# Optimization experiments

Measured on AMD Instinct MI355X. Metric: run time of the kernel, lower is better.

Reference implementation:

```python
import jax, jax.numpy as jnp
import numpy as np

VOCAB = 32000
HIDDEN = 1024
BATCH = 8
SEQ = 512


def setup_inputs() -> dict:
    key = jax.random.key(0)
    ks = jax.random.split(key, 6)
    scale = 1.0 / np.sqrt(HIDDEN)
    return {
        "sequence_ids": jax.random.randint(ks[0], (BATCH, SEQ), 0, VOCAB, dtype=jnp.int64),
        "W_out": jax.random.normal(ks[1], (HIDDEN, VOCAB), dtype=jnp.float32) * scale,
        "b_out": jax.random.normal(ks[2], (VOCAB,), dtype=jnp.float32) * 0.01,
        "Wx": jax.random.normal(ks[3], (HIDDEN, 4 * HIDDEN), dtype=jnp.float32) * scale,
        "Wh": jax.random.normal(ks[4], (HIDDEN, 4 * HIDDEN), dtype=jnp.float32) * scale,
        "b_lstm": jax.random.normal(ks[5], (4 * HIDDEN,), dtype=jnp.float32) * 0.01,
    }


def _lstm(emb, Wx, Wh, b):
    # emb: [B, S, H]; scan over time with carry (h, c) of shape [B, H]
    B, S, H = emb.shape
    # Precompute input projections for all timesteps in one big GEMM.
    x_gates = jnp.einsum("bsh,hg->bsg", emb, Wx) + b  # [B, S, 4H]

    def step(carry, xg_t):
        h, c = carry
        gates = xg_t + h @ Wh  # [B, 4H]
        i, f, g, o = jnp.split(gates, 4, axis=-1)
        i = jax.nn.sigmoid(i)
        f = jax.nn.sigmoid(f)
        g = jnp.tanh(g)
        o = jax.nn.sigmoid(o)
        c = f * c + i * g
        h = o * jnp.tanh(c)
        return (h, c), h

    h0 = jnp.zeros((B, H), dtype=emb.dtype)
    c0 = jnp.zeros((B, H), dtype=emb.dtype)
    (_, _), hs = jax.lax.scan(step, (h0, c0), jnp.swapaxes(x_gates, 0, 1))
    return jnp.swapaxes(hs, 0, 1)  # [B, S, H]


def reference(sequence_ids, W_out, b_out, Wx, Wh, b_lstm):
    # Weight-tied embedding lookup: W_out is [H, V]; take columns -> [B, S, H]
    emb = W_out.T[sequence_ids]
    hs = _lstm(emb, Wx, Wh, b_lstm)  # [B, S, H]
    logits = jnp.einsum("bsh,hv->bsv", hs, W_out) + b_out  # [B, S, V]
    return logits
```

## Files before the change

kernel.cpp:

```cpp
#include <hip/hip_runtime.h>

#define VOCAB  32000
#define HIDDEN 1024
#define BATCH  8
#define SEQ    512
#define GDIM   4096

typedef short bf16x8 __attribute__((ext_vector_type(8)));
typedef float f32x4  __attribute__((ext_vector_type(4)));

__device__ __forceinline__ unsigned short f2bf(float f) {
    unsigned int u = __float_as_uint(f);
    u += 0x7fff + ((u >> 16) & 1);
    return (unsigned short)(u >> 16);
}

__device__ __forceinline__ float sigmoidf_(float x) {
    return 1.0f / (1.0f + expf(-x));
}

__global__ __launch_bounds__(256) void convert_bf16(const float* __restrict__ in,
                                                    unsigned short* __restrict__ out,
                                                    int n4) {
    int i = blockIdx.x * 256 + threadIdx.x;
    if (i < n4) {
        float4 v = ((const float4*)in)[i];
        ushort4 o;
        o.x = f2bf(v.x); o.y = f2bf(v.y); o.z = f2bf(v.z); o.w = f2bf(v.w);
        ((ushort4*)out)[i] = o;
    }
}

__global__ __launch_bounds__(256) void gather_emb(const int* __restrict__ ids,
                                                  const float* __restrict__ W_out,
                                                  unsigned short* __restrict__ emb) {
    int r = blockIdx.x;
    int s = r >> 3, b = r & 7;
    int v = ids[b * SEQ + s];
    #pragma unroll
    for (int i = 0; i < 4; ++i) {
        int h = threadIdx.x + i * 256;
        emb[r * HIDDEN + h] = f2bf(W_out[(size_t)h * VOCAB + v]);
    }
}

__global__ __launch_bounds__(256) void transpose_wh(const float* __restrict__ Wh,
                                                    unsigned short* __restrict__ whT) {
    __shared__ unsigned short tile[32][33];
    const int j0 = blockIdx.x * 32;
    const int k0 = blockIdx.y * 32;
    const int c = threadIdx.x & 31;
    const int r = threadIdx.x >> 5;
    #pragma unroll
    for (int i = 0; i < 4; ++i) {
        int rr = r + i * 8;
        tile[rr][c] = f2bf(Wh[(size_t)(k0 + rr) * GDIM + j0 + c]);
    }
    __syncthreads();
    #pragma unroll
    for (int i = 0; i < 4; ++i) {
        int rr = r + i * 8;
        whT[(size_t)(j0 + rr) * HIDDEN + k0 + c] = tile[c][rr];
    }
}

__global__ __launch_bounds__(256) void gemm_bf16_bias(
        const unsigned short* __restrict__ A,
        const unsigned short* __restrict__ B,
        const float* __restrict__ bias,
        float* __restrict__ C,
        int M, int N, int K) {
    __shared__ __attribute__((aligned(16))) unsigned short As[128 * 40];
    __shared__ __attribute__((aligned(16))) unsigned short Bs[128 * 40];

    const int tid  = threadIdx.x;
    const int lane = tid & 63;
    const int wave = tid >> 6;
    const int wm = wave >> 1, wn = wave & 1;
    const int quad = lane >> 4, r16 = lane & 15;
    const int m0 = blockIdx.y * 128, n0 = blockIdx.x * 128;

    f32x4 acc[4][4] = {};

    for (int k0 = 0; k0 < K; k0 += 32) {
        #pragma unroll
        for (int i = 0; i < 2; ++i) {
            int c = tid + 256 * i;
            int m = c >> 2, kc = (c & 3) * 8;
            uint4 v = *(const uint4*)(A + (size_t)(m0 + m) * K + k0 + kc);
            *(uint4*)(As + m * 40 + kc) = v;
        }
        #pragma unroll
        for (int i = 0; i < 2; ++i) {
            int c = tid + 256 * i;
            int k = c >> 4, nc = (c & 15) * 8;
            uint4 v = *(const uint4*)(B + (size_t)(k0 + k) * N + n0 + nc);
            union { uint4 q; unsigned short s[8]; } u; u.q = v;
            #pragma unroll
            for (int j = 0; j < 8; ++j) Bs[(nc + j) * 40 + k] = u.s[j];
        }
        __syncthreads();

        bf16x8 af[4], bfr[4];
        #pragma unroll
        for (int mi = 0; mi < 4; ++mi)
            af[mi] = *(const bf16x8*)(As + (wm * 64 + mi * 16 + r16) * 40 + quad * 8);
        #pragma unroll
        for (int ni = 0; ni < 4; ++ni)
            bfr[ni] = *(const bf16x8*)(Bs + (wn * 64 + ni * 16 + r16) * 40 + quad * 8);

        #pragma unroll
        for (int mi = 0; mi < 4; ++mi)
            #pragma unroll
            for (int ni = 0; ni < 4; ++ni)
                acc[mi][ni] = __builtin_amdgcn_mfma_f32_16x16x32_bf16(
                    af[mi], bfr[ni], acc[mi][ni], 0, 0, 0);
        __syncthreads();
    }

    #pragma unroll
    for (int mi = 0; mi < 4; ++mi) {
        #pragma unroll
        for (int ni = 0; ni < 4; ++ni) {
            int col = n0 + wn * 64 + ni * 16 + r16;
            float bv = bias[col];
            #pragma unroll
            for (int r = 0; r < 4; ++r) {
                int row = m0 + wm * 64 + mi * 16 + quad * 4 + r;
                C[(size_t)row * N + col] = acc[mi][ni][r] + bv;
            }
        }
    }
}

__global__ __launch_bounds__(256) void lstm_step_mfma(
        const float* __restrict__ xg,
        const unsigned short* __restrict__ whT,
        const unsigned short* __restrict__ h_in,
        unsigned short* __restrict__ h_out,
        float* __restrict__ c,
        unsigned short* __restrict__ hs,
        int t) {
    __shared__ float sg[4][8][16];

    const int tid  = threadIdx.x;
    const int lane = tid & 63;
    const int g    = tid >> 6;
    const int r16  = lane & 15;
    const int quad = lane >> 4;
    const int u0   = blockIdx.x * 16;
    const int j0   = g * HIDDEN + u0;

    f32x4 acc = {};
    const unsigned short* ap = h_in + r16 * HIDDEN + quad * 8;
    const unsigned short* bp = whT + (size_t)(j0 + r16) * HIDDEN + quad * 8;
    #pragma unroll 16
    for (int kk = 0; kk < HIDDEN / 32; ++kk) {
        bf16x8 af = *(const bf16x8*)(ap + kk * 32);
        bf16x8 bf = *(const bf16x8*)(bp + kk * 32);
        acc = __builtin_amdgcn_mfma_f32_16x16x32_bf16(af, bf, acc, 0, 0, 0);
    }

    if (quad < 2) {
        const float* xp = xg + (size_t)(t * BATCH) * GDIM + j0 + r16;
        #pragma unroll
        for (int r = 0; r < 4; ++r) {
            int row = quad * 4 + r;
            sg[g][row][r16] = acc[r] + xp[(size_t)row * GDIM];
        }
    }
    __syncthreads();

    if (tid < 128) {
        int b = tid >> 4, ui = tid & 15, u = u0 + ui;
        float iv = sigmoidf_(sg[0][b][ui]);
        float fv = sigmoidf_(sg[1][b][ui]);
        float gv = tanhf(sg[2][b][ui]);
        float ov = sigmoidf_(sg[3][b][ui]);
        float cn = fv * c[b * HIDDEN + u] + iv * gv;
        c[b * HIDDEN + u] = cn;
        float hv = ov * tanhf(cn);
        unsigned short hb = f2bf(hv);
        h_out[b * HIDDEN + u] = hb;
        hs[((size_t)b * SEQ + t) * HIDDEN + u] = hb;
    }
}

extern "C" void kernel_launch(void* const* d_in, const int* in_sizes, int n_in,
                              void* d_out, int out_size, void* d_ws, size_t ws_size,
                              hipStream_t stream) {
    const int*   ids    = (const int*)d_in[0];
    const float* W_out  = (const float*)d_in[1];
    const float* b_out  = (const float*)d_in[2];
    const float* Wx     = (const float*)d_in[3];
    const float* Wh     = (const float*)d_in[4];
    const float* b_lstm = (const float*)d_in[5];
    float* out = (float*)d_out;

    char* ws = (char*)d_ws;
    float*          xg     = (float*)(ws + 0);
    unsigned short* emb    = (unsigned short*)(ws + 67108864);
    unsigned short* whT    = (unsigned short*)(ws + 67108864);
    unsigned short* wx16   = (unsigned short*)(ws + 75497472);
    unsigned short* wout16 = (unsigned short*)(ws + 83886080);
    unsigned short* hs16   = (unsigned short*)(ws + 149422080);
    unsigned short* h16    = (unsigned short*)(ws + 157810688);
    float*          cbuf   = (float*)(ws + 157876224);

    hipMemsetAsync(h16, 0, 65536 + 32768, stream);

    convert_bf16<<<(HIDDEN * GDIM / 4 + 255) / 256, 256, 0, stream>>>(Wx, wx16, HIDDEN * GDIM / 4);
    convert_bf16<<<(HIDDEN * VOCAB / 4 + 255) / 256, 256, 0, stream>>>(W_out, wout16, HIDDEN * VOCAB / 4);

    gather_emb<<<SEQ * BATCH, 256, 0, stream>>>(ids, W_out, emb);

    gemm_bf16_bias<<<dim3(GDIM / 128, SEQ * BATCH / 128), 256, 0, stream>>>(
        emb, wx16, b_lstm, xg, SEQ * BATCH, GDIM, HIDDEN);

    transpose_wh<<<dim3(GDIM / 32, HIDDEN / 32), 256, 0, stream>>>(Wh, whT);

    for (int t = 0; t < SEQ; ++t) {
        const unsigned short* hin = h16 + (t & 1) * (16 * HIDDEN);
        unsigned short* hout      = h16 + ((t + 1) & 1) * (16 * HIDDEN);
        lstm_step_mfma<<<HIDDEN / 16, 256, 0, stream>>>(xg, whT, hin, hout, cbuf, hs16, t);
    }

    gemm_bf16_bias<<<dim3(VOCAB / 128, SEQ * BATCH / 128), 256, 0, stream>>>(
        hs16, wout16, b_out, out, SEQ * BATCH, VOCAB, HIDDEN);
}
```

Before: 7.077 ms.

## Fuse LSTM time loop into persistent cooperative kernel with grid barrier

Replaces 512 per-timestep kernel launches with one cooperative persistent kernel of 64 blocks that loops over time and synchronises through an atomic grid barrier. Each block keeps its Wh slice in registers and holds the cell state in a register, so weights are not reloaded every step and the c buffer round trip is gone. The MFMA reduction is split across four accumulators to shorten the dependency chain. The embedding gather now reads the already converted bf16 W_out. The cost is register pressure from the 32 resident weight vectors, and correctness relies on the spin barrier and on all blocks being co-resident.

```diff
diff --git a/kernel.cpp b/kernel.cpp
--- a/kernel.cpp
+++ b/kernel.cpp
@@ -5,6 +5,7 @@
 #define BATCH  8
 #define SEQ    512
 #define GDIM   4096
+#define NBLK   64
 
 typedef short bf16x8 __attribute__((ext_vector_type(8)));
 typedef float f32x4  __attribute__((ext_vector_type(4)));
@@ -32,7 +33,7 @@
 }
 
 __global__ __launch_bounds__(256) void gather_emb(const int* __restrict__ ids,
-                                                  const float* __restrict__ W_out,
+                                                  const unsigned short* __restrict__ w16,
                                                   unsigned short* __restrict__ emb) {
     int r = blockIdx.x;
     int s = r >> 3, b = r & 7;
@@ -40,7 +41,7 @@
     #pragma unroll
     for (int i = 0; i < 4; ++i) {
         int h = threadIdx.x + i * 256;
-        emb[r * HIDDEN + h] = f2bf(W_out[(size_t)h * VOCAB + v]);
+        emb[r * HIDDEN + h] = w16[(size_t)h * VOCAB + v];
     }
 }
 
@@ -133,14 +134,25 @@
     }
 }
 
-__global__ __launch_bounds__(256) void lstm_step_mfma(
+__device__ __forceinline__ void grid_sync(unsigned* bar) {
+    __syncthreads();
+    if (threadIdx.x == 0) {
+        __threadfence();
+        unsigned token  = atomicAdd(bar, 1u) + 1u;
+        unsigned target = ((token + NBLK - 1u) / NBLK) * NBLK;
+        while (__hip_atomic_load(bar, __ATOMIC_RELAXED, __HIP_MEMORY_SCOPE_AGENT) < target)
+            __builtin_amdgcn_s_sleep(2);
+        __threadfence();
+    }
+    __syncthreads();
+}
+
+__global__ __launch_bounds__(256) void lstm_scan(
         const float* __restrict__ xg,
         const unsigned short* __restrict__ whT,
-        const unsigned short* __restrict__ h_in,
-        unsigned short* __restrict__ h_out,
-        float* __restrict__ c,
+        unsigned short* __restrict__ h_buf,
         unsigned short* __restrict__ hs,
-        int t) {
+        unsigned* __restrict__ bar) {
     __shared__ float sg[4][8][16];
 
     const int tid  = threadIdx.x;
@@ -151,38 +163,65 @@
     const int u0   = blockIdx.x * 16;
     const int j0   = g * HIDDEN + u0;
 
-    f32x4 acc = {};
-    const unsigned short* ap = h_in + r16 * HIDDEN + quad * 8;
-    const unsigned short* bp = whT + (size_t)(j0 + r16) * HIDDEN + quad * 8;
-    #pragma unroll 16
-    for (int kk = 0; kk < HIDDEN / 32; ++kk) {
-        bf16x8 af = *(const bf16x8*)(ap + kk * 32);
-        bf16x8 bf = *(const bf16x8*)(bp + kk * 32);
-        acc = __builtin_amdgcn_mfma_f32_16x16x32_bf16(af, bf, acc, 0, 0, 0);
-    }
-
-    if (quad < 2) {
-        const float* xp = xg + (size_t)(t * BATCH) * GDIM + j0 + r16;
-        #pragma unroll
-        for (int r = 0; r < 4; ++r) {
-            int row = quad * 4 + r;
-            sg[g][row][r16] = acc[r] + xp[(size_t)row * GDIM];
-        }
-    }
-    __syncthreads();
-
-    if (tid < 128) {
-        int b = tid >> 4, ui = tid & 15, u = u0 + ui;
-        float iv = sigmoidf_(sg[0][b][ui]);
-        float fv = sigmoidf_(sg[1][b][ui]);
-        float gv = tanhf(sg[2][b][ui]);
-        float ov = sigmoidf_(sg[3][b][ui]);
-        float cn = fv * c[b * HIDDEN + u] + iv * gv;
-        c[b * HIDDEN + u] = cn;
-        float hv = ov * tanhf(cn);
-        unsigned short hb = f2bf(hv);
-        h_out[b * HIDDEN + u] = hb;
-        hs[((size_t)b * SEQ + t) * HIDDEN + u] = hb;
+    bf16x8 bw[32];
+    {
+        const unsigned short* bp = whT + (size_t)(j0 + r16) * HIDDEN + quad * 8;
+        #pragma unroll
+        for (int kk = 0; kk < 32; ++kk)
+            bw[kk] = *(const bf16x8*)(bp + kk * 32);
+    }
+
+    float creg = 0.0f;
+    const int pb = tid >> 4, pu = tid & 15;
+
+    for (int t = 0; t < SEQ; ++t) {
+        const unsigned short* hb = h_buf + (t & 1) * (16 * HIDDEN);
+        unsigned short* hn       = h_buf + ((t + 1) & 1) * (16 * HIDDEN);
+
+        float xv[4];
+        if (quad < 2) {
+            const float* xp = xg + (size_t)t * BATCH * GDIM + j0 + r16;
+            #pragma unroll
+            for (int r = 0; r < 4; ++r)
+                xv[r] = xp[(size_t)(quad * 4 + r) * GDIM];
+        }
+
+        const unsigned short* ap = hb + r16 * HIDDEN + quad * 8;
+        f32x4 ac0 = {}, ac1 = {}, ac2 = {}, ac3 = {};
+        #pragma unroll
+        for (int kk = 0; kk < 32; kk += 4) {
+            bf16x8 a0 = *(const bf16x8*)(ap + (kk + 0) * 32);
+            bf16x8 a1 = *(const bf16x8*)(ap + (kk + 1) * 32);
+            bf16x8 a2 = *(const bf16x8*)(ap + (kk + 2) * 32);
+            bf16x8 a3 = *(const bf16x8*)(ap + (kk + 3) * 32);
+            ac0 = __builtin_amdgcn_mfma_f32_16x16x32_bf16(a0, bw[kk + 0], ac0, 0, 0, 0);
+            ac1 = __builtin_amdgcn_mfma_f32_16x16x32_bf16(a1, bw[kk + 1], ac1, 0, 0, 0);
+            ac2 = __builtin_amdgcn_mfma_f32_16x16x32_bf16(a2, bw[kk + 2], ac2, 0, 0, 0);
+            ac3 = __builtin_amdgcn_mfma_f32_16x16x32_bf16(a3, bw[kk + 3], ac3, 0, 0, 0);
+        }
+        f32x4 acc = (ac0 + ac1) + (ac2 + ac3);
+
+        if (quad < 2) {
+            #pragma unroll
+            for (int r = 0; r < 4; ++r)
+                sg[g][quad * 4 + r][r16] = acc[r] + xv[r];
+        }
+        __syncthreads();
+
+        if (tid < 128) {
+            float iv = sigmoidf_(sg[0][pb][pu]);
+            float fv = sigmoidf_(sg[1][pb][pu]);
+            float gv = tanhf(sg[2][pb][pu]);
+            float ov = sigmoidf_(sg[3][pb][pu]);
+            creg = fv * creg + iv * gv;
+            float hv = ov * tanhf(creg);
+            unsigned short hbf = f2bf(hv);
+            int u = u0 + pu;
+            hn[pb * HIDDEN + u] = hbf;
+            hs[((size_t)pb * SEQ + t) * HIDDEN + u] = hbf;
+        }
+
+        grid_sync(bar);
     }
 }
 
@@ -205,24 +244,30 @@
     unsigned short* wout16 = (unsigned short*)(ws + 83886080);
     unsigned short* hs16   = (unsigned short*)(ws + 149422080);
     unsigned short* h16    = (unsigned short*)(ws + 157810688);
-    float*          cbuf   = (float*)(ws + 157876224);
-
-    hipMemsetAsync(h16, 0, 65536 + 32768, stream);
+    unsigned*       bar    = (unsigned*)(ws + 157876224);
+
+    hipMemsetAsync(h16, 0, 65536 + 4096, stream);
 
     convert_bf16<<<(HIDDEN * GDIM / 4 + 255) / 256, 256, 0, stream>>>(Wx, wx16, HIDDEN * GDIM / 4);
     convert_bf16<<<(HIDDEN * VOCAB / 4 + 255) / 256, 256, 0, stream>>>(W_out, wout16, HIDDEN * VOCAB / 4);
 
-    gather_emb<<<SEQ * BATCH, 256, 0, stream>>>(ids, W_out, emb);
+    gather_emb<<<SEQ * BATCH, 256, 0, stream>>>(ids, wout16, emb);
 
     gemm_bf16_bias<<<dim3(GDIM / 128, SEQ * BATCH / 128), 256, 0, stream>>>(
         emb, wx16, b_lstm, xg, SEQ * BATCH, GDIM, HIDDEN);
 
     transpose_wh<<<dim3(GDIM / 32, HIDDEN / 32), 256, 0, stream>>>(Wh, whT);
 
-    for (int t = 0; t < SEQ; ++t) {
-        const unsigned short* hin = h16 + (t & 1) * (16 * HIDDEN);
-        unsigned short* hout      = h16 + ((t + 1) & 1) * (16 * HIDDEN);
-        lstm_step_mfma<<<HIDDEN / 16, 256, 0, stream>>>(xg, whT, hin, hout, cbuf, hs16, t);
+    {
+        const float* xg_c = xg;
+        const unsigned short* whT_c = whT;
+        unsigned short* h16_p = h16;
+        unsigned short* hs_p  = hs16;
+        unsigned* bar_p = bar;
+        void* args[] = { (void*)&xg_c, (void*)&whT_c, (void*)&h16_p,
+                         (void*)&hs_p, (void*)&bar_p };
+        hipLaunchCooperativeKernel((void*)lstm_scan, dim3(NBLK), dim3(256),
+                                   args, 0, stream);
     }
 
     gemm_bf16_bias<<<dim3(VOCAB / 128, SEQ * BATCH / 128), 256, 0, stream>>>(
```

Measured after the change: 7.976 ms. 12.7% more time.
